# Kernel optimization log

Hardware: AMD Instinct MI355X
Metric: run time of the kernel (lower is better)

The kernel has to match this reference:

```python
import jax, jax.numpy as jnp
import numpy as np

B, N, D, H = 8, 1024, 1024, 16
DH = D // H
EPS = 1e-6


def setup_inputs() -> dict:
    key = jax.random.key(0)
    ks = jax.random.split(key, 12)
    s = 1.0 / np.sqrt(D)
    inp = {
        "x": jax.random.normal(ks[0], (B, N, D), jnp.float32),
        "y": jax.random.normal(ks[1], (B, N, D), jnp.float32),
        "Wq": jax.random.normal(ks[2], (D, D), jnp.float32) * s,
        "bq": jnp.zeros((D,), jnp.float32),
        "Wk": jax.random.normal(ks[3], (D, D), jnp.float32) * s,
        "bk": jnp.zeros((D,), jnp.float32),
        "Wv": jax.random.normal(ks[4], (D, D), jnp.float32) * s,
        "bv": jnp.zeros((D,), jnp.float32),
        "Wf": jax.random.normal(ks[5], (D, D), jnp.float32) * s,
        "bf": jnp.zeros((D,), jnp.float32),
        "g1": jnp.ones((D,), jnp.float32),
        "b1": jnp.zeros((D,), jnp.float32),
        "g2": jnp.ones((D,), jnp.float32),
        "b2": jnp.zeros((D,), jnp.float32),
    }
    return inp


def _layernorm(x, g, b):
    mu = jnp.mean(x, axis=-1, keepdims=True)
    var = jnp.mean(jnp.square(x - mu), axis=-1, keepdims=True)
    return (x - mu) * jax.lax.rsqrt(var + EPS) * g + b


def reference(x, y, Wq, bq, Wk, bk, Wv, bv, Wf, bf, g1, b1, g2, b2):
    q = x @ Wq + bq                      # [B, Nq, D]
    k = y @ Wk + bk                      # [B, Nk, D]
    v = y @ Wv + bv                      # [B, Nk, D]
    qh = q.reshape(B, N, H, DH)
    kh = k.reshape(B, N, H, DH)
    vh = v.reshape(B, N, H, DH)
    # NOTE: original scales by sqrt(embed_dim), not sqrt(head_dim)
    scores = jnp.einsum("bqhd,bkhd->bhqk", qh, kh) / jnp.sqrt(jnp.float32(D))
    att = jax.nn.softmax(scores, axis=-1)
    o = jnp.einsum("bhqk,bkhd->bqhd", att, vh).reshape(B, N, D)
    out = x + o
    out = _layernorm(out, g1, b1)
    out = out + jax.nn.relu(out @ Wf + bf)
    out = _layernorm(out, g2, b2)
    return out
```

## Files before the change

kernel.cpp:

```cpp
#include <hip/hip_runtime.h>


#define Bb 8
#define Nn 1024
#define Dd 1024
#define Hh 16
#define DH 64
#define Mrows (Bb * Nn)

#define QSCL 0.045084220027780106f

typedef float f32x4 __attribute__((ext_vector_type(4)));
typedef __bf16 bf16x8 __attribute__((ext_vector_type(8)));
typedef unsigned int u32x4 __attribute__((ext_vector_type(4)));

#define MFMA16(acc, a, b) \
  acc = __builtin_amdgcn_mfma_f32_16x16x32_bf16((a), (b), (acc), 0, 0, 0)

__device__ __forceinline__ bf16x8 ld_frag(const void* p) {
  u32x4 v = *(const u32x4*)p;
  return __builtin_bit_cast(bf16x8, v);
}

__device__ __forceinline__ void gload16(const void* g, void* l) {
  __builtin_amdgcn_global_load_lds(
      (const __attribute__((address_space(1))) unsigned int*)g,
      (__attribute__((address_space(3))) unsigned int*)l, 16, 0, 0);
}

__device__ __forceinline__ unsigned short f2bf(float f) {
  return __builtin_bit_cast(unsigned short, (__bf16)f);
}
__device__ __forceinline__ float bf2f(unsigned short s) {
  unsigned int u = ((unsigned int)s) << 16;
  return __builtin_bit_cast(float, u);
}

__global__ __launch_bounds__(256) void cvt_f32_bf16_2(
    const float* __restrict__ in0, unsigned short* __restrict__ out0,
    const float* __restrict__ in1, unsigned short* __restrict__ out1, int n4) {
  const float* in = blockIdx.y ? in1 : in0;
  unsigned short* out = blockIdx.y ? out1 : out0;
  int i = blockIdx.x * blockDim.x + threadIdx.x;
  int stride = gridDim.x * blockDim.x;
  for (; i < n4; i += stride) {
    float4 v = ((const float4*)in)[i];
    ushort4 o;
    o.x = f2bf(v.x); o.y = f2bf(v.y); o.z = f2bf(v.z); o.w = f2bf(v.w);
    ((ushort4*)out)[i] = o;
  }
}

__global__ __launch_bounds__(256) void transpose_cvt4(
    const float* __restrict__ W0, const float* __restrict__ W1,
    const float* __restrict__ W2, const float* __restrict__ W3,
    unsigned short* __restrict__ T0, unsigned short* __restrict__ T1,
    unsigned short* __restrict__ T2, unsigned short* __restrict__ T3) {
  __shared__ float tile[32][33];
  const float* W = blockIdx.z == 0 ? W0 : blockIdx.z == 1 ? W1
                   : blockIdx.z == 2 ? W2 : W3;
  unsigned short* Wt = blockIdx.z == 0 ? T0 : blockIdx.z == 1 ? T1
                       : blockIdx.z == 2 ? T2 : T3;
  int tx = threadIdx.x, ty = threadIdx.y;
  int n0 = blockIdx.x * 32, k0 = blockIdx.y * 32;
#pragma unroll
  for (int i = ty; i < 32; i += 8)
    tile[i][tx] = W[(size_t)(k0 + i) * Dd + n0 + tx];
  __syncthreads();
#pragma unroll
  for (int i = ty; i < 32; i += 8)
    Wt[(size_t)(n0 + i) * Dd + k0 + tx] = f2bf(tile[tx][i]);
}

template <int EPI>
__global__ __launch_bounds__(256) void gemm_bt(
    const unsigned short* __restrict__ A, const unsigned short* __restrict__ Bt,
    const float* __restrict__ bias, unsigned short* __restrict__ Cb,
    const unsigned short* __restrict__ Tres,
    unsigned short* __restrict__ VtOut, int M, int N, int K) {
  __shared__ __attribute__((aligned(16))) unsigned short As[2][128 * 32];
  __shared__ __attribute__((aligned(16))) unsigned short Bs[2][128 * 32];
  const int bid = blockIdx.y * 8 + blockIdx.x;
  const int nwg = (gridDim.x * gridDim.y);
  const int swz = (bid & 7) * (nwg >> 3) + (bid >> 3);
  const int m0 = (swz >> 3) * 128, n0 = (swz & 7) * 128;
  const int t = threadIdx.x, w = t >> 6, l = t & 63;
  const int wm = (w >> 1) * 64, wn = (w & 1) * 64;
  const int lr = l & 15, lk = (l >> 4) * 8;
  const int rA = t >> 2, sA = (t & 3) * 8;
  char* AsB = (char*)As;
  char* BsB = (char*)Bs;
  const int wb = (w * 64) * 16;

  f32x4 acc[4][4] = {};

  for (int k0 = 0; k0 < K; k0 += 64) {
    __syncthreads();
#pragma unroll
    for (int h = 0; h < 2; ++h) {
      const int ko = k0 + h * 32;
      gload16(A + (size_t)(m0 + rA) * K + ko + sA, AsB + h * 8192 + wb);
      gload16(A + (size_t)(m0 + 64 + rA) * K + ko + sA, AsB + h * 8192 + wb + 4096);
      gload16(Bt + (size_t)(n0 + rA) * K + ko + sA, BsB + h * 8192 + wb);
      gload16(Bt + (size_t)(n0 + 64 + rA) * K + ko + sA, BsB + h * 8192 + wb + 4096);
    }
    __syncthreads();

#pragma unroll
    for (int h = 0; h < 2; ++h) {
      bf16x8 af[4], bfr[4];
#pragma unroll
      for (int i = 0; i < 4; ++i)
        af[i] = ld_frag(&As[h][(wm + i * 16 + lr) * 32 + lk]);
#pragma unroll
      for (int j = 0; j < 4; ++j)
        bfr[j] = ld_frag(&Bs[h][(wn + j * 16 + lr) * 32 + lk]);
#pragma unroll
      for (int i = 0; i < 4; ++i)
#pragma unroll
        for (int j = 0; j < 4; ++j) MFMA16(acc[i][j], af[i], bfr[j]);
    }
  }

  const int lg = l >> 4;
#pragma unroll
  for (int i = 0; i < 4; ++i)
#pragma unroll
    for (int j = 0; j < 4; ++j) {
      int col = n0 + wn + j * 16 + lr;
      float bcol = bias[col];
      if (EPI == 2) {
        int brow = m0 + wm + i * 16 + lg * 4;
        int bi = brow >> 10, nloc = brow & 1023;
        ushort4 o4;
        o4.x = f2bf(acc[i][j][0] + bcol);
        o4.y = f2bf(acc[i][j][1] + bcol);
        o4.z = f2bf(acc[i][j][2] + bcol);
        o4.w = f2bf(acc[i][j][3] + bcol);
        *(ushort4*)(VtOut + ((size_t)bi * Dd + col) * Nn + nloc) = o4;
      } else {
#pragma unroll
        for (int r = 0; r < 4; ++r) {
          int row = m0 + wm + i * 16 + lg * 4 + r;
          float v = acc[i][j][r] + bcol;
          size_t idx = (size_t)row * N + col;
          if (EPI == 0) {
            Cb[idx] = f2bf(v);
          } else if (EPI == 3) {
            Cb[idx] = f2bf(v * QSCL);
          } else {
            Cb[idx] = f2bf(bf2f(Tres[idx]) + fmaxf(v, 0.f));
          }
        }
      }
    }
}

__global__ __launch_bounds__(256) void attn_fwd(
    const unsigned short* __restrict__ Qg, const unsigned short* __restrict__ Kg,
    const unsigned short* __restrict__ Vt, unsigned short* __restrict__ Obf) {
  __shared__ __attribute__((aligned(16))) unsigned short Ks[64 * 64];
  __shared__ __attribute__((aligned(16))) unsigned short Vts[64 * 64];
  __shared__ __attribute__((aligned(16))) unsigned short Ps[128 * 64];
  char* KsB = (char*)Ks;
  char* VtsB = (char*)Vts;
  char* PsB = (char*)Ps;

  const int bid = blockIdx.y * 8 + blockIdx.x;
  const int swz = (bid & 7) * 128 + (bid >> 3);
  const int q0 = (swz & 7) * 128;
  const int by = swz >> 3;
  const int b = by >> 4, h = by & 15;

  const int t = threadIdx.x, w = t >> 6, l = t & 63;
  const int lr = l & 15, lg = l >> 4;

  bf16x8 aq[2][2];
#pragma unroll
  for (int i = 0; i < 2; ++i) {
    const unsigned short* qp =
        Qg + ((size_t)b * Nn + q0 + w * 32 + i * 16 + lr) * Dd + h * DH + lg * 8;
    aq[i][0] = *(const bf16x8*)qp;
    aq[i][1] = *(const bf16x8*)(qp + 32);
  }

  const size_t baseK = (size_t)b * Nn * Dd + h * DH;
  const size_t baseV = ((size_t)b * Dd + h * DH) * Nn;

  const int srow = t >> 3, sch = t & 7;
  const int sby = srow * 128 + ((sch * 16) ^ ((srow & 7) << 4));
  const int sby2 = sby + 32 * 128;

  uint4 kA = *(const uint4*)(Kg + baseK + (size_t)srow * Dd + sch * 8);
  uint4 kB = *(const uint4*)(Kg + baseK + (size_t)(srow + 32) * Dd + sch * 8);
  uint4 vA = *(const uint4*)(Vt + baseV + (size_t)srow * Nn + sch * 8);
  uint4 vB = *(const uint4*)(Vt + baseV + (size_t)(srow + 32) * Nn + sch * 8);

  f32x4 oacc[2][4] = {};
  float lp[2][4] = {};

  const int fx = (lg * 16) ^ ((lr & 7) << 4);

  for (int kv = 0; kv < Nn / 64; ++kv) {
    __syncthreads();
    *(uint4*)(KsB + sby) = kA;
    *(uint4*)(KsB + sby2) = kB;
    *(uint4*)(VtsB + sby) = vA;
    *(uint4*)(VtsB + sby2) = vB;
    __syncthreads();

    if (kv + 1 < Nn / 64) {
      int kvo = (kv + 1) * 64;
      kA = *(const uint4*)(Kg + baseK + (size_t)(kvo + srow) * Dd + sch * 8);
      kB = *(const uint4*)(Kg + baseK + (size_t)(kvo + srow + 32) * Dd + sch * 8);
      vA = *(const uint4*)(Vt + baseV + (size_t)srow * Nn + kvo + sch * 8);
      vB = *(const uint4*)(Vt + baseV + (size_t)(srow + 32) * Nn + kvo + sch * 8);
    }

    f32x4 sacc[2][4];
    __builtin_amdgcn_s_setprio(1);
#pragma unroll
    for (int j = 0; j < 4; ++j) {
      const int kro = (j * 16 + lr) * 128;
      bf16x8 b0 = ld_frag(KsB + kro + fx);
      bf16x8 b1 = ld_frag(KsB + kro + (fx ^ 64));
#pragma unroll
      for (int i = 0; i < 2; ++i) {
        f32x4 z = {0.f, 0.f, 0.f, 0.f};
        MFMA16(z, aq[i][0], b0);
        MFMA16(z, aq[i][1], b1);
        sacc[i][j] = z;
      }
    }
    __builtin_amdgcn_s_setprio(0);

#pragma unroll
    for (int i = 0; i < 2; ++i)
#pragma unroll
      for (int rr = 0; rr < 4; ++rr) {
        float e0 = exp2f(sacc[i][0][rr]);
        float e1 = exp2f(sacc[i][1][rr]);
        float e2 = exp2f(sacc[i][2][rr]);
        float e3 = exp2f(sacc[i][3][rr]);
        lp[i][rr] += (e0 + e1) + (e2 + e3);
        int prow = w * 32 + i * 16 + lg * 4 + rr;
        char* pb = PsB + prow * 128;
        int px = (prow & 7) << 4;
        *(unsigned short*)(pb + ((2 * lr) ^ px)) = f2bf(e0);
        *(unsigned short*)(pb + ((32 + 2 * lr) ^ px)) = f2bf(e1);
        *(unsigned short*)(pb + ((64 + 2 * lr) ^ px)) = f2bf(e2);
        *(unsigned short*)(pb + ((96 + 2 * lr) ^ px)) = f2bf(e3);
      }

    asm volatile("s_waitcnt lgkmcnt(0)" ::: "memory");
    __builtin_amdgcn_sched_barrier(0);

    bf16x8 ap[2][2];
#pragma unroll
    for (int i = 0; i < 2; ++i) {
      const int aro = (w * 32 + i * 16 + lr) * 128;
      ap[i][0] = ld_frag(PsB + aro + fx);
      ap[i][1] = ld_frag(PsB + aro + (fx ^ 64));
    }
    __builtin_amdgcn_s_setprio(1);
#pragma unroll
    for (int j = 0; j < 4; ++j) {
      const int vro = (j * 16 + lr) * 128;
      bf16x8 bv0 = ld_frag(VtsB + vro + fx);
      bf16x8 bv1 = ld_frag(VtsB + vro + (fx ^ 64));
#pragma unroll
      for (int i = 0; i < 2; ++i) {
        MFMA16(oacc[i][j], ap[i][0], bv0);
        MFMA16(oacc[i][j], ap[i][1], bv1);
      }
    }
    __builtin_amdgcn_s_setprio(0);
  }

  float rdiv[2][4];
#pragma unroll
  for (int i = 0; i < 2; ++i)
#pragma unroll
    for (int rr = 0; rr < 4; ++rr) {
      float s = lp[i][rr];
#pragma unroll
      for (int o = 1; o < 16; o <<= 1) s += __shfl_xor(s, o, 64);
      rdiv[i][rr] = 1.f / s;
    }
#pragma unroll
  for (int i = 0; i < 2; ++i)
#pragma unroll
    for (int j = 0; j < 4; ++j)
#pragma unroll
      for (int rr = 0; rr < 4; ++rr) {
        int row = q0 + w * 32 + i * 16 + lg * 4 + rr;
        int col = h * DH + j * 16 + lr;
        Obf[((size_t)b * Nn + row) * Dd + col] =
            f2bf(oacc[i][j][rr] * rdiv[i][rr]);
      }
}

template <int MODE>
__global__ __launch_bounds__(256) void ln_k(
    const unsigned short* __restrict__ X, const unsigned short* __restrict__ Oin,
    const float* __restrict__ gamma, const float* __restrict__ beta,
    unsigned short* __restrict__ out_bf, float* __restrict__ out_f) {
  __shared__ float red[8];
  const int row = blockIdx.x, t = threadIdx.x;
  ushort4 xu = ((const ushort4*)(X + (size_t)row * Dd))[t];
  float4 v = {bf2f(xu.x), bf2f(xu.y), bf2f(xu.z), bf2f(xu.w)};
  if (MODE == 0) {
    ushort4 o = ((const ushort4*)(Oin + (size_t)row * Dd))[t];
    v.x += bf2f(o.x); v.y += bf2f(o.y); v.z += bf2f(o.z); v.w += bf2f(o.w);
  }
  float s = v.x + v.y + v.z + v.w;
#pragma unroll
  for (int o = 32; o > 0; o >>= 1) s += __shfl_xor(s, o, 64);
  if ((t & 63) == 0) red[t >> 6] = s;
  __syncthreads();
  float mean = (red[0] + red[1] + red[2] + red[3]) * (1.f / 1024.f);
  float dx = v.x - mean, dy = v.y - mean, dz = v.z - mean, dw = v.w - mean;
  float s2 = dx * dx + dy * dy + dz * dz + dw * dw;
#pragma unroll
  for (int o = 32; o > 0; o >>= 1) s2 += __shfl_xor(s2, o, 64);
  if ((t & 63) == 0) red[4 + (t >> 6)] = s2;
  __syncthreads();
  float var = (red[4] + red[5] + red[6] + red[7]) * (1.f / 1024.f);
  float rstd = rsqrtf(var + 1e-6f);
  float4 g = ((const float4*)gamma)[t];
  float4 bb = ((const float4*)beta)[t];
  float r0 = dx * rstd * g.x + bb.x;
  float r1 = dy * rstd * g.y + bb.y;
  float r2 = dz * rstd * g.z + bb.z;
  float r3 = dw * rstd * g.w + bb.w;
  if (MODE == 0) {
    ushort4 o4;
    o4.x = f2bf(r0); o4.y = f2bf(r1); o4.z = f2bf(r2); o4.w = f2bf(r3);
    ((ushort4*)(out_bf + (size_t)row * Dd))[t] = o4;
  } else {
    float4 o4 = {r0, r1, r2, r3};
    ((float4*)(out_f + (size_t)row * Dd))[t] = o4;
  }
}

extern "C" void kernel_launch(void* const* d_in, const int* in_sizes, int n_in,
                              void* d_out, int out_size, void* d_ws, size_t ws_size,
                              hipStream_t stream) {
  const float* x  = (const float*)d_in[0];
  const float* y  = (const float*)d_in[1];
  const float* Wq = (const float*)d_in[2];
  const float* bq = (const float*)d_in[3];
  const float* Wk = (const float*)d_in[4];
  const float* bk = (const float*)d_in[5];
  const float* Wv = (const float*)d_in[6];
  const float* bv = (const float*)d_in[7];
  const float* Wf = (const float*)d_in[8];
  const float* bf = (const float*)d_in[9];
  const float* g1 = (const float*)d_in[10];
  const float* b1 = (const float*)d_in[11];
  const float* g2 = (const float*)d_in[12];
  const float* b2 = (const float*)d_in[13];

  char* ws = (char*)d_ws;
  const size_t MB = 1024 * 1024;
  unsigned short* xb  = (unsigned short*)(ws + 0 * MB);
  unsigned short* yb  = (unsigned short*)(ws + 16 * MB);
  unsigned short* WqT = (unsigned short*)(ws + 32 * MB);
  unsigned short* WkT = (unsigned short*)(ws + 34 * MB);
  unsigned short* WvT = (unsigned short*)(ws + 36 * MB);
  unsigned short* WfT = (unsigned short*)(ws + 38 * MB);
  unsigned short* Qb  = (unsigned short*)(ws + 40 * MB);
  unsigned short* Kb  = (unsigned short*)(ws + 56 * MB);
  unsigned short* Vtb = (unsigned short*)(ws + 72 * MB);
  unsigned short* Obf = (unsigned short*)(ws + 16 * MB);
  unsigned short* tb  = (unsigned short*)(ws + 40 * MB);
  unsigned short* ub  = (unsigned short*)(ws + 56 * MB);

  const int n4 = (Mrows * Dd) / 4;
  cvt_f32_bf16_2<<<dim3(1024, 2), 256, 0, stream>>>(x, xb, y, yb, n4);

  transpose_cvt4<<<dim3(32, 32, 4), dim3(32, 8), 0, stream>>>(
      Wq, Wk, Wv, Wf, WqT, WkT, WvT, WfT);

  dim3 gg(Dd / 128, Mrows / 128);
  gemm_bt<3><<<gg, 256, 0, stream>>>(xb, WqT, bq, Qb, nullptr, nullptr, Mrows, Dd, Dd);
  gemm_bt<0><<<gg, 256, 0, stream>>>(yb, WkT, bk, Kb, nullptr, nullptr, Mrows, Dd, Dd);
  gemm_bt<2><<<gg, 256, 0, stream>>>(yb, WvT, bv, nullptr, nullptr, Vtb, Mrows, Dd, Dd);

  attn_fwd<<<dim3(Nn / 128, Bb * Hh), 256, 0, stream>>>(Qb, Kb, Vtb, Obf);

  ln_k<0><<<Mrows, 256, 0, stream>>>(xb, Obf, g1, b1, tb, nullptr);

  gemm_bt<1><<<gg, 256, 0, stream>>>(tb, WfT, bf, ub, tb, nullptr, Mrows, Dd, Dd);

  ln_k<1><<<Mrows, 256, 0, stream>>>(ub, nullptr, g2, b2, nullptr, (float*)d_out);
}
```

Measured before the change: 226.2 us.

## Merge QKV GEMMs into one launch and keep attention probabilities in registers

The three Q/K/V projection GEMMs now run as a single launch with a z grid dimension, sharing a templated GEMM core with lambda epilogues. The attention kernel computes transposed scores (K as the A operand), so the exponentiated probabilities already sit in the B-operand layout of the PV MFMA. They are packed to bf16 with v_cvt_pk_bf16_f32 and used directly, which removes the LDS round trip for P, its barrier/waitcnt, and the per-row shuffle reductions. In exchange, V is read from LDS as split 8-byte loads, and the output is written in a transposed accumulator layout.

```diff
diff --git a/kernel.cpp b/kernel.cpp
--- a/kernel.cpp
+++ b/kernel.cpp
@@ -6,7 +6,7 @@
 #define Dd 1024
 #define Hh 16
 #define DH 64
-#define Mrows (Bb * Nn)
+#define Mrows (Bb * 1024)
 
 #define QSCL 0.045084220027780106f
 
@@ -34,6 +34,11 @@
 __device__ __forceinline__ float bf2f(unsigned short s) {
   unsigned int u = ((unsigned int)s) << 16;
   return __builtin_bit_cast(float, u);
+}
+__device__ __forceinline__ unsigned cvt_pk_bf16(float a, float b) {
+  unsigned r;
+  asm("v_cvt_pk_bf16_f32 %0, %1, %2" : "=v"(r) : "v"(a), "v"(b));
+  return r;
 }
 
 __global__ __launch_bounds__(256) void cvt_f32_bf16_2(
@@ -72,12 +77,12 @@
     Wt[(size_t)(n0 + i) * Dd + k0 + tx] = f2bf(tile[tx][i]);
 }
 
-template <int EPI>
-__global__ __launch_bounds__(256) void gemm_bt(
+struct GemmCtx { int m0, n0, wm, wn, lr, lk, lg, l, w; };
+
+template <typename EpiFn>
+__device__ __forceinline__ void gemm_core(
     const unsigned short* __restrict__ A, const unsigned short* __restrict__ Bt,
-    const float* __restrict__ bias, unsigned short* __restrict__ Cb,
-    const unsigned short* __restrict__ Tres,
-    unsigned short* __restrict__ VtOut, int M, int N, int K) {
+    int K, EpiFn epi) {
   __shared__ __attribute__((aligned(16))) unsigned short As[2][128 * 32];
   __shared__ __attribute__((aligned(16))) unsigned short Bs[2][128 * 32];
   const int bid = blockIdx.y * 8 + blockIdx.x;
@@ -121,39 +126,71 @@
         for (int j = 0; j < 4; ++j) MFMA16(acc[i][j], af[i], bfr[j]);
     }
   }
-
-  const int lg = l >> 4;
-#pragma unroll
-  for (int i = 0; i < 4; ++i)
-#pragma unroll
-    for (int j = 0; j < 4; ++j) {
-      int col = n0 + wn + j * 16 + lr;
-      float bcol = bias[col];
-      if (EPI == 2) {
-        int brow = m0 + wm + i * 16 + lg * 4;
-        int bi = brow >> 10, nloc = brow & 1023;
-        ushort4 o4;
-        o4.x = f2bf(acc[i][j][0] + bcol);
-        o4.y = f2bf(acc[i][j][1] + bcol);
-        o4.z = f2bf(acc[i][j][2] + bcol);
-        o4.w = f2bf(acc[i][j][3] + bcol);
-        *(ushort4*)(VtOut + ((size_t)bi * Dd + col) * Nn + nloc) = o4;
-      } else {
-#pragma unroll
-        for (int r = 0; r < 4; ++r) {
-          int row = m0 + wm + i * 16 + lg * 4 + r;
-          float v = acc[i][j][r] + bcol;
-          size_t idx = (size_t)row * N + col;
-          if (EPI == 0) {
-            Cb[idx] = f2bf(v);
-          } else if (EPI == 3) {
-            Cb[idx] = f2bf(v * QSCL);
-          } else {
-            Cb[idx] = f2bf(bf2f(Tres[idx]) + fmaxf(v, 0.f));
+  GemmCtx c{m0, n0, wm, wn, lr, lk, l >> 4, l, w};
+  epi(acc, c);
+}
+
+__global__ __launch_bounds__(256) void gemm_qkv(
+    const unsigned short* __restrict__ xb, const unsigned short* __restrict__ yb,
+    const unsigned short* __restrict__ WqT, const unsigned short* __restrict__ WkT,
+    const unsigned short* __restrict__ WvT,
+    const float* __restrict__ bq, const float* __restrict__ bk,
+    const float* __restrict__ bv,
+    unsigned short* __restrict__ Qb, unsigned short* __restrict__ Kb,
+    unsigned short* __restrict__ Vtb) {
+  const int z = blockIdx.z;
+  const unsigned short* A = (z == 0) ? xb : yb;
+  const unsigned short* Bt = (z == 0) ? WqT : (z == 1) ? WkT : WvT;
+  const float* bias = (z == 0) ? bq : (z == 1) ? bk : bv;
+  unsigned short* Cb = (z == 0) ? Qb : Kb;
+
+  gemm_core(A, Bt, Dd, [&](f32x4 (&acc)[4][4], GemmCtx c) {
+#pragma unroll
+    for (int i = 0; i < 4; ++i)
+#pragma unroll
+      for (int j = 0; j < 4; ++j) {
+        int col = c.n0 + c.wn + j * 16 + c.lr;
+        float bcol = bias[col];
+        if (z == 2) {
+          int brow = c.m0 + c.wm + i * 16 + c.lg * 4;
+          int bi = brow >> 10, nloc = brow & 1023;
+          ushort4 o4;
+          o4.x = f2bf(acc[i][j][0] + bcol);
+          o4.y = f2bf(acc[i][j][1] + bcol);
+          o4.z = f2bf(acc[i][j][2] + bcol);
+          o4.w = f2bf(acc[i][j][3] + bcol);
+          *(ushort4*)(Vtb + ((size_t)bi * Dd + col) * Nn + nloc) = o4;
+        } else {
+          float scl = (z == 0) ? QSCL : 1.0f;
+#pragma unroll
+          for (int r = 0; r < 4; ++r) {
+            int row = c.m0 + c.wm + i * 16 + c.lg * 4 + r;
+            Cb[(size_t)row * Dd + col] = f2bf((acc[i][j][r] + bcol) * scl);
           }
         }
       }
-    }
+  });
+}
+
+__global__ __launch_bounds__(256) void gemm_ff(
+    const unsigned short* __restrict__ A, const unsigned short* __restrict__ Bt,
+    const float* __restrict__ bias, const unsigned short* __restrict__ Tres,
+    unsigned short* __restrict__ Cb) {
+  gemm_core(A, Bt, Dd, [&](f32x4 (&acc)[4][4], GemmCtx c) {
+#pragma unroll
+    for (int i = 0; i < 4; ++i)
+#pragma unroll
+      for (int j = 0; j < 4; ++j) {
+        int col = c.n0 + c.wn + j * 16 + c.lr;
+        float bcol = bias[col];
+#pragma unroll
+        for (int r = 0; r < 4; ++r) {
+          int row = c.m0 + c.wm + i * 16 + c.lg * 4 + r;
+          size_t idx = (size_t)row * Dd + col;
+          Cb[idx] = f2bf(bf2f(Tres[idx]) + fmaxf(acc[i][j][r] + bcol, 0.f));
+        }
+      }
+  });
 }
 
 __global__ __launch_bounds__(256) void attn_fwd(
@@ -161,10 +198,8 @@
     const unsigned short* __restrict__ Vt, unsigned short* __restrict__ Obf) {
   __shared__ __attribute__((aligned(16))) unsigned short Ks[64 * 64];
   __shared__ __attribute__((aligned(16))) unsigned short Vts[64 * 64];
-  __shared__ __attribute__((aligned(16))) unsigned short Ps[128 * 64];
   char* KsB = (char*)Ks;
   char* VtsB = (char*)Vts;
-  char* PsB = (char*)Ps;
 
   const int bid = blockIdx.y * 8 + blockIdx.x;
   const int swz = (bid & 7) * 128 + (bid >> 3);
@@ -196,8 +231,8 @@
   uint4 vA = *(const uint4*)(Vt + baseV + (size_t)srow * Nn + sch * 8);
   uint4 vB = *(const uint4*)(Vt + baseV + (size_t)(srow + 32) * Nn + sch * 8);
 
-  f32x4 oacc[2][4] = {};
-  float lp[2][4] = {};
+  f32x4 oacc[4][2] = {};
+  float lp[2] = {0.f, 0.f};
 
   const int fx = (lg * 16) ^ ((lr & 7) << 4);
 
@@ -217,87 +252,84 @@
       vB = *(const uint4*)(Vt + baseV + (size_t)(srow + 32) * Nn + kvo + sch * 8);
     }
 
-    f32x4 sacc[2][4];
+    f32x4 st[2][4];
     __builtin_amdgcn_s_setprio(1);
 #pragma unroll
     for (int j = 0; j < 4; ++j) {
       const int kro = (j * 16 + lr) * 128;
-      bf16x8 b0 = ld_frag(KsB + kro + fx);
-      bf16x8 b1 = ld_frag(KsB + kro + (fx ^ 64));
+      bf16x8 k0 = ld_frag(KsB + kro + fx);
+      bf16x8 k1 = ld_frag(KsB + kro + (fx ^ 64));
 #pragma unroll
       for (int i = 0; i < 2; ++i) {
         f32x4 z = {0.f, 0.f, 0.f, 0.f};
-        MFMA16(z, aq[i][0], b0);
-        MFMA16(z, aq[i][1], b1);
-        sacc[i][j] = z;
+        MFMA16(z, k0, aq[i][0]);
+        MFMA16(z, k1, aq[i][1]);
+        st[i][j] = z;
       }
     }
     __builtin_amdgcn_s_setprio(0);
 
 #pragma unroll
-    for (int i = 0; i < 2; ++i)
-#pragma unroll
-      for (int rr = 0; rr < 4; ++rr) {
-        float e0 = exp2f(sacc[i][0][rr]);
-        float e1 = exp2f(sacc[i][1][rr]);
-        float e2 = exp2f(sacc[i][2][rr]);
-        float e3 = exp2f(sacc[i][3][rr]);
-        lp[i][rr] += (e0 + e1) + (e2 + e3);
-        int prow = w * 32 + i * 16 + lg * 4 + rr;
-        char* pb = PsB + prow * 128;
-        int px = (prow & 7) << 4;
-        *(unsigned short*)(pb + ((2 * lr) ^ px)) = f2bf(e0);
-        *(unsigned short*)(pb + ((32 + 2 * lr) ^ px)) = f2bf(e1);
-        *(unsigned short*)(pb + ((64 + 2 * lr) ^ px)) = f2bf(e2);
-        *(unsigned short*)(pb + ((96 + 2 * lr) ^ px)) = f2bf(e3);
-      }
-
-    asm volatile("s_waitcnt lgkmcnt(0)" ::: "memory");
-    __builtin_amdgcn_sched_barrier(0);
-
-    bf16x8 ap[2][2];
-#pragma unroll
     for (int i = 0; i < 2; ++i) {
-      const int aro = (w * 32 + i * 16 + lr) * 128;
-      ap[i][0] = ld_frag(PsB + aro + fx);
-      ap[i][1] = ld_frag(PsB + aro + (fx ^ 64));
-    }
-    __builtin_amdgcn_s_setprio(1);
-#pragma unroll
-    for (int j = 0; j < 4; ++j) {
-      const int vro = (j * 16 + lr) * 128;
-      bf16x8 bv0 = ld_frag(VtsB + vro + fx);
-      bf16x8 bv1 = ld_frag(VtsB + vro + (fx ^ 64));
+      float s = 0.f;
+#pragma unroll
+      for (int j = 0; j < 4; ++j) {
+        float e0 = exp2f(st[i][j][0]);
+        float e1 = exp2f(st[i][j][1]);
+        float e2 = exp2f(st[i][j][2]);
+        float e3 = exp2f(st[i][j][3]);
+        st[i][j][0] = e0; st[i][j][1] = e1; st[i][j][2] = e2; st[i][j][3] = e3;
+        s += (e0 + e1) + (e2 + e3);
+      }
+      lp[i] += s;
+    }
+
+#pragma unroll
+    for (int m = 0; m < 2; ++m) {
+      bf16x8 pb[2];
 #pragma unroll
       for (int i = 0; i < 2; ++i) {
-        MFMA16(oacc[i][j], ap[i][0], bv0);
-        MFMA16(oacc[i][j], ap[i][1], bv1);
-      }
-    }
-    __builtin_amdgcn_s_setprio(0);
-  }
-
-  float rdiv[2][4];
-#pragma unroll
-  for (int i = 0; i < 2; ++i)
-#pragma unroll
-    for (int rr = 0; rr < 4; ++rr) {
-      float s = lp[i][rr];
-#pragma unroll
-      for (int o = 1; o < 16; o <<= 1) s += __shfl_xor(s, o, 64);
-      rdiv[i][rr] = 1.f / s;
-    }
-#pragma unroll
-  for (int i = 0; i < 2; ++i)
-#pragma unroll
-    for (int j = 0; j < 4; ++j)
-#pragma unroll
-      for (int rr = 0; rr < 4; ++rr) {
-        int row = q0 + w * 32 + i * 16 + lg * 4 + rr;
-        int col = h * DH + j * 16 + lr;
-        Obf[((size_t)b * Nn + row) * Dd + col] =
-            f2bf(oacc[i][j][rr] * rdiv[i][rr]);
-      }
+        u32x4 pk;
+        pk[0] = cvt_pk_bf16(st[i][2 * m][0], st[i][2 * m][1]);
+        pk[1] = cvt_pk_bf16(st[i][2 * m][2], st[i][2 * m][3]);
+        pk[2] = cvt_pk_bf16(st[i][2 * m + 1][0], st[i][2 * m + 1][1]);
+        pk[3] = cvt_pk_bf16(st[i][2 * m + 1][2], st[i][2 * m + 1][3]);
+        pb[i] = __builtin_bit_cast(bf16x8, pk);
+      }
+      __builtin_amdgcn_s_setprio(1);
+#pragma unroll
+      for (int da = 0; da < 4; ++da) {
+        const int vrow = da * 16 + lr;
+        const int vbase = vrow * 128;
+        const int vswz = (vrow & 7) << 4;
+        uint2 a0 = *(const uint2*)(VtsB + vbase + ((64 * m + 8 * lg) ^ vswz));
+        uint2 a1 = *(const uint2*)(VtsB + vbase + ((64 * m + 32 + 8 * lg) ^ vswz));
+        u32x4 av = {a0.x, a0.y, a1.x, a1.y};
+        bf16x8 va = __builtin_bit_cast(bf16x8, av);
+        MFMA16(oacc[da][0], va, pb[0]);
+        MFMA16(oacc[da][1], va, pb[1]);
+      }
+      __builtin_amdgcn_s_setprio(0);
+    }
+  }
+
+#pragma unroll
+  for (int i = 0; i < 2; ++i) {
+    float s = lp[i];
+    s += __shfl_xor(s, 16, 64);
+    s += __shfl_xor(s, 32, 64);
+    float rd = 1.f / s;
+    const size_t orow = (size_t)b * Nn + q0 + w * 32 + i * 16 + lr;
+#pragma unroll
+    for (int da = 0; da < 4; ++da) {
+      ushort4 o4;
+      o4.x = f2bf(oacc[da][i][0] * rd);
+      o4.y = f2bf(oacc[da][i][1] * rd);
+      o4.z = f2bf(oacc[da][i][2] * rd);
+      o4.w = f2bf(oacc[da][i][3] * rd);
+      *(ushort4*)(Obf + orow * Dd + h * DH + da * 16 + lg * 4) = o4;
+    }
+  }
 }
 
 template <int MODE>
@@ -382,16 +414,14 @@
   transpose_cvt4<<<dim3(32, 32, 4), dim3(32, 8), 0, stream>>>(
       Wq, Wk, Wv, Wf, WqT, WkT, WvT, WfT);
 
-  dim3 gg(Dd / 128, Mrows / 128);
-  gemm_bt<3><<<gg, 256, 0, stream>>>(xb, WqT, bq, Qb, nullptr, nullptr, Mrows, Dd, Dd);
-  gemm_bt<0><<<gg, 256, 0, stream>>>(yb, WkT, bk, Kb, nullptr, nullptr, Mrows, Dd, Dd);
-  gemm_bt<2><<<gg, 256, 0, stream>>>(yb, WvT, bv, nullptr, nullptr, Vtb, Mrows, Dd, Dd);
-
-  attn_fwd<<<dim3(Nn / 128, Bb * Hh), 256, 0, stream>>>(Qb, Kb, Vtb, Obf);
+  gemm_qkv<<<dim3(8, 64, 3), 256, 0, stream>>>(
+      xb, yb, WqT, WkT, WvT, bq, bk, bv, Qb, Kb, Vtb);
+
+  attn_fwd<<<dim3(8, 128), 256, 0, stream>>>(Qb, Kb, Vtb, Obf);
 
   ln_k<0><<<Mrows, 256, 0, stream>>>(xb, Obf, g1, b1, tb, nullptr);
 
-  gemm_bt<1><<<gg, 256, 0, stream>>>(tb, WfT, bf, ub, tb, nullptr, Mrows, Dd, Dd);
+  gemm_ff<<<dim3(8, 64), 256, 0, stream>>>(tb, WfT, bf, tb, ub);
 
   ln_k<1><<<Mrows, 256, 0, stream>>>(ub, nullptr, g2, b2, nullptr, (float*)d_out);
 }
```

Measured after the change: 216.2 us. 1.05x faster.
